# Kernel optimization log

Hardware: AMD Instinct MI355X
Metric: run time of the kernel (lower is better)

Reference implementation:

```python
import jax, jax.numpy as jnp
import numpy as np

N_NODES = 50000
N_EDGES = 800000
NFEAT = 512
NHID = 64
NHEADS = 8
NCLASS = 40
ALPHA = 0.2  # LeakyReLU slope
EPS = 1e-16  # guards isolated-node division


def setup_inputs() -> dict:
    key = jax.random.key(0)
    k = jax.random.split(key, 6)
    x = jax.random.normal(k[0], (N_NODES, NFEAT), dtype=jnp.float32)
    W_heads = jax.random.normal(k[1], (NHEADS, NFEAT, NHID), dtype=jnp.float32) * 0.05
    a_heads = jax.random.normal(k[2], (NHEADS, 2 * NHID), dtype=jnp.float32) * 0.05
    W_out = jax.random.normal(k[3], (NHEADS * NHID, NCLASS), dtype=jnp.float32) * 0.05
    a_out = jax.random.normal(k[4], (2 * NCLASS,), dtype=jnp.float32) * 0.05
    edge_index = jax.random.randint(k[5], (2, N_EDGES), 0, N_NODES, dtype=jnp.int32)
    return {"x": x, "W_heads": W_heads, "a_heads": a_heads,
            "W_out": W_out, "a_out": a_out, "edge_index": edge_index}


def _gat_layer(x, W, a, row, col, concat):
    # pyGAT sparse layer: h = xW; e_ij = exp(-LeakyReLU(a^T [h_i || h_j]));
    # out_i = sum_j e_ij h_j / sum_j e_ij   (aggregate into row, gather from col)
    D = W.shape[1]
    h = x @ W                                            # [N, D]
    score = h[row] @ a[:D] + h[col] @ a[D:]              # [E]
    e = jnp.exp(-jax.nn.leaky_relu(score, ALPHA))        # [E]
    num = jax.ops.segment_sum(e[:, None] * h[col], row, num_segments=x.shape[0])  # [N, D]
    den = jax.ops.segment_sum(e, row, num_segments=x.shape[0])                    # [N]
    out = num / (den[:, None] + EPS)
    return jax.nn.elu(out) if concat else out


def reference(x, W_heads, a_heads, W_out, a_out, edge_index):
    # dropout layers are identity in eval mode (training=False)
    row, col = edge_index[0], edge_index[1]
    heads = jax.vmap(lambda W, a: _gat_layer(x, W, a, row, col, True))(W_heads, a_heads)
    # [H, N, D] -> [N, H*D] (concat along feature dim, head-major like torch.cat)
    hcat = jnp.transpose(heads, (1, 0, 2)).reshape(x.shape[0], -1)
    return _gat_layer(hcat, W_out, a_out, row, col, False)  # [N, NCLASS]
```

## Files before the change

kernel.cpp:

```cpp
#include <hip/hip_runtime.h>
#include <hip/hip_bf16.h>

#define N_NODES 50000
#define N_EDGES 800000
#define NFEAT   512
#define NHID    64
#define NHEADS  8
#define NCLASS  40
#define HD      (NHEADS*NHID)
#define ALPHA   0.2f
#define EPS_F   1e-16f
#define NCHUNK  ((N_NODES + 255)/256)

typedef __attribute__((ext_vector_type(8))) short short8;
typedef __attribute__((ext_vector_type(4))) float floatx4;

__device__ __forceinline__ float bf2f(unsigned short u) {
    union { unsigned int i; float f; } v; v.i = ((unsigned int)u) << 16; return v.f;
}
__device__ __forceinline__ unsigned short f2bf(float f) {
    union { __hip_bfloat16 h; unsigned short u; } cv;
    cv.h = __float2bfloat16(f);
    return cv.u;
}

__global__ void prep(const float* __restrict__ Wh, unsigned short* __restrict__ Wrb,
                     const float* __restrict__ Wo, unsigned short* __restrict__ Wob,
                     int* __restrict__ deg) {
    int idx = blockIdx.x*256 + threadIdx.x;
    if (idx >= 512*512) return;
    if (idx < N_NODES) deg[idx] = 0;
    {
        int n = idx >> 9, k = idx & 511;
        int hd = n >> 6, d = n & 63;
        Wrb[idx] = f2bf(Wh[(size_t)hd*NFEAT*NHID + (size_t)k*NHID + d]);
    }
    if (idx < 64*512) {
        int n = idx >> 9, k = idx & 511;
        float v = (n < NCLASS) ? Wo[(size_t)k*NCLASS + n] : 0.f;
        Wob[idx] = f2bf(v);
    }
}

__global__ __launch_bounds__(512, 4) void mfma_gemm1(const float* __restrict__ A,
                                                  const unsigned short* __restrict__ Bbf,
                                                  const float* __restrict__ a_heads,
                                                  unsigned short* __restrict__ H1p,
                                                  float* __restrict__ srcdot,
                                                  float* __restrict__ dstdot, int M) {
    int id = blockIdx.x;
    int rb = (id >> 5)*8 + (id & 7);
    int cb = (id >> 3) & 3;
    int row0 = rb * 128, col0 = cb * 128;
    if (row0 >= M) return;

    __shared__ short Asl[128*40];
    __shared__ short Bsl[128*40];
    int tid  = threadIdx.x;
    int wid  = tid >> 6, lane = tid & 63;
    int lrow = lane & 15, quad = lane >> 4;
    int wm = wid >> 1, wn = wid & 1;

    int sr = tid >> 2, sk = (tid & 3) * 8;
    int ar = row0 + sr;
    int arow = ar < M ? ar : M - 1;

    floatx4 acc[2][4];
#pragma unroll
    for (int mm = 0; mm < 2; mm++)
#pragma unroll
        for (int nn = 0; nn < 4; nn++) acc[mm][nn] = (floatx4){0.f,0.f,0.f,0.f};

    float4 fa0, fa1;
    short8 fb;
    {
        const float* src = A + (size_t)arow*512 + sk;
        fa0 = *(const float4*)src;
        fa1 = *(const float4*)(src + 4);
        fb  = *(const short8*)(Bbf + (size_t)(col0 + sr)*512 + sk);
    }

    for (int k0 = 0; k0 < 512; k0 += 32) {
        {
            short8 h;
            h[0] = (short)f2bf(fa0.x); h[1] = (short)f2bf(fa0.y);
            h[2] = (short)f2bf(fa0.z); h[3] = (short)f2bf(fa0.w);
            h[4] = (short)f2bf(fa1.x); h[5] = (short)f2bf(fa1.y);
            h[6] = (short)f2bf(fa1.z); h[7] = (short)f2bf(fa1.w);
            *(short8*)(&Asl[sr*40 + sk]) = h;
            *(short8*)(&Bsl[sr*40 + sk]) = fb;
        }
        __syncthreads();
        if (k0 + 32 < 512) {
            int kn = k0 + 32;
            const float* src = A + (size_t)arow*512 + kn + sk;
            fa0 = *(const float4*)src;
            fa1 = *(const float4*)(src + 4);
            fb  = *(const short8*)(Bbf + (size_t)(col0 + sr)*512 + kn + sk);
        }
        short8 af[2], bfr[4];
#pragma unroll
        for (int mm = 0; mm < 2; ++mm)
            af[mm] = *(const short8*)(&Asl[(wm*32 + mm*16 + lrow)*40 + quad*8]);
#pragma unroll
        for (int nn = 0; nn < 4; ++nn)
            bfr[nn] = *(const short8*)(&Bsl[(wn*64 + nn*16 + lrow)*40 + quad*8]);
#pragma unroll
        for (int mm = 0; mm < 2; ++mm)
#pragma unroll
            for (int nn = 0; nn < 4; ++nn)
                acc[mm][nn] = __builtin_amdgcn_mfma_f32_16x16x32_bf16(
                    af[mm], bfr[nn], acc[mm][nn], 0, 0, 0);
        __syncthreads();
    }

    {
        int head = (col0 >> 6) + wn;
        float a0v[4], a1v[4];
#pragma unroll
        for (int nn = 0; nn < 4; ++nn) {
            a0v[nn] = a_heads[head*128 + nn*16 + lrow];
            a1v[nn] = a_heads[head*128 + 64 + nn*16 + lrow];
        }
#pragma unroll
        for (int mm = 0; mm < 2; ++mm) {
#pragma unroll
            for (int r = 0; r < 4; ++r) {
                float s0 = 0.f, s1 = 0.f;
#pragma unroll
                for (int nn = 0; nn < 4; ++nn) {
                    float v = acc[mm][nn][r];
                    s0 = fmaf(v, a0v[nn], s0);
                    s1 = fmaf(v, a1v[nn], s1);
                }
#pragma unroll
                for (int off = 1; off < 16; off <<= 1) {
                    s0 += __shfl_xor(s0, off, 64);
                    s1 += __shfl_xor(s1, off, 64);
                }
                int grow = row0 + wm*32 + mm*16 + quad*4 + r;
                if (lrow == 0 && grow < M) {
                    srcdot[(size_t)grow*8 + head] = s0;
                    dstdot[(size_t)grow*8 + head] = s1;
                }
            }
        }
    }

#pragma unroll
    for (int mm = 0; mm < 2; ++mm) {
        int rbase = row0 + wm*32 + mm*16 + quad*4;
#pragma unroll
        for (int nn = 0; nn < 4; ++nn) {
            int c = col0 + wn*64 + nn*16 + lrow;
            int off = (c & 63)*8 + (c >> 6);
#pragma unroll
            for (int r = 0; r < 4; ++r) {
                int grow = rbase + r;
                if (grow < M)
                    H1p[(size_t)grow*512 + off] = f2bf(acc[mm][nn][r]);
            }
        }
    }
}

__global__ __launch_bounds__(512, 4) void mfma_gemm2(const unsigned short* __restrict__ Abf,
                                                  const unsigned short* __restrict__ Bbf,
                                                  const float* __restrict__ a_out,
                                                  float* __restrict__ H2p,
                                                  float* __restrict__ src2,
                                                  float* __restrict__ dst2, int M) {
    __shared__ short Asl[128*40];
    __shared__ short Bsl[64*40];
    int tid  = threadIdx.x;
    int wid  = tid >> 6, lane = tid & 63;
    int lrow = lane & 15, quad = lane >> 4;
    int row0 = blockIdx.x * 128;
    if (row0 >= M) return;

    int sr = tid >> 2, sk = (tid & 3) * 8;
    int ar = row0 + sr; ar = ar < M ? ar : M - 1;
    int sr2 = (tid & 255) >> 2, sk2 = (tid & 3) * 8;

    floatx4 acc[4];
#pragma unroll
    for (int nn = 0; nn < 4; nn++) acc[nn] = (floatx4){0.f,0.f,0.f,0.f};

    short8 fa, fbv;
    fa = *(const short8*)(Abf + (size_t)ar*512 + sk);
    if (tid < 256)
        fbv = *(const short8*)(Bbf + (size_t)sr2*512 + sk2);

    for (int k0 = 0; k0 < 512; k0 += 32) {
        *(short8*)(&Asl[sr*40 + sk]) = fa;
        if (tid < 256)
            *(short8*)(&Bsl[sr2*40 + sk2]) = fbv;
        __syncthreads();
        if (k0 + 32 < 512) {
            int kn = k0 + 32;
            fa = *(const short8*)(Abf + (size_t)ar*512 + kn + sk);
            if (tid < 256)
                fbv = *(const short8*)(Bbf + (size_t)sr2*512 + kn + sk2);
        }
        short8 af, bfr[4];
        af = *(const short8*)(&Asl[(wid*16 + lrow)*40 + quad*8]);
#pragma unroll
        for (int nn = 0; nn < 4; ++nn)
            bfr[nn] = *(const short8*)(&Bsl[(nn*16 + lrow)*40 + quad*8]);
#pragma unroll
        for (int nn = 0; nn < 4; ++nn)
            acc[nn] = __builtin_amdgcn_mfma_f32_16x16x32_bf16(
                af, bfr[nn], acc[nn], 0, 0, 0);
        __syncthreads();
    }

    {
        float a0v[4], a1v[4];
#pragma unroll
        for (int nn = 0; nn < 4; ++nn) {
            int c = nn*16 + lrow;
            a0v[nn] = c < NCLASS ? a_out[c] : 0.f;
            a1v[nn] = c < NCLASS ? a_out[NCLASS + c] : 0.f;
        }
#pragma unroll
        for (int r = 0; r < 4; ++r) {
            float s0 = 0.f, s1 = 0.f;
#pragma unroll
            for (int nn = 0; nn < 4; ++nn) {
                float v = acc[nn][r];
                s0 = fmaf(v, a0v[nn], s0);
                s1 = fmaf(v, a1v[nn], s1);
            }
#pragma unroll
            for (int off = 1; off < 16; off <<= 1) {
                s0 += __shfl_xor(s0, off, 64);
                s1 += __shfl_xor(s1, off, 64);
            }
            int grow = row0 + wid*16 + quad*4 + r;
            if (lrow == 0 && grow < M) {
                src2[grow] = s0;
                dst2[grow] = s1;
            }
        }
    }

#pragma unroll
    for (int nn = 0; nn < 4; ++nn) {
        int c = nn*16 + lrow;
#pragma unroll
        for (int r = 0; r < 4; ++r) {
            int grow = row0 + wid*16 + quad*4 + r;
            if (grow < M)
                H2p[(size_t)grow*64 + c] = acc[nn][r];
        }
    }
}

__global__ void histk(const int* __restrict__ row, int* __restrict__ deg) {
    int e = blockIdx.x*256 + threadIdx.x;
    if (e < N_EDGES) atomicAdd(&deg[row[e]], 1);
}
__global__ void scanA(const int* __restrict__ deg, int* __restrict__ row_ptr,
                      int* __restrict__ chunk_tot) {
    __shared__ int s[256];
    int t = threadIdx.x;
    int idx = blockIdx.x*256 + t;
    int v = (idx < N_NODES) ? deg[idx] : 0;
    s[t] = v;
    __syncthreads();
#pragma unroll
    for (int off = 1; off < 256; off <<= 1) {
        int x = (t >= off) ? s[t-off] : 0;
        __syncthreads();
        s[t] += x;
        __syncthreads();
    }
    if (idx < N_NODES) row_ptr[idx] = s[t] - v;
    if (t == 255) chunk_tot[blockIdx.x] = s[t];
}
__global__ void scanB(const int* __restrict__ chunk_tot, int* __restrict__ chunk_off,
                      int* __restrict__ row_ptr) {
    __shared__ int s[256];
    int t = threadIdx.x;
    int v = (t < NCHUNK) ? chunk_tot[t] : 0;
    s[t] = v;
    __syncthreads();
#pragma unroll
    for (int off = 1; off < 256; off <<= 1) {
        int x = (t >= off) ? s[t-off] : 0;
        __syncthreads();
        s[t] += x;
        __syncthreads();
    }
    if (t < NCHUNK) chunk_off[t] = s[t] - v;
    if (t == 255) row_ptr[N_NODES] = s[t];
}
__global__ void scanC(const int* __restrict__ chunk_off, int* __restrict__ row_ptr,
                      int* __restrict__ cursor) {
    int idx = blockIdx.x*256 + threadIdx.x;
    if (idx < N_NODES) {
        int rp = row_ptr[idx] + chunk_off[idx >> 8];
        row_ptr[idx] = rp;
        cursor[idx] = rp;
    }
}

__global__ void fillk_w1(const int* __restrict__ row, const int* __restrict__ col,
                         const float* __restrict__ srcdot, const float* __restrict__ dstdot,
                         int* __restrict__ cursor, int* __restrict__ csr_col,
                         float* __restrict__ Wcsr) {
    int e = blockIdx.x*256 + threadIdx.x;
    if (e >= N_EDGES) return;
    int r = row[e], c = col[e];
    int pos = atomicAdd(&cursor[r], 1);
    csr_col[pos] = c;
    float4 sa = *(const float4*)(srcdot + (size_t)r*8);
    float4 sb = *(const float4*)(srcdot + (size_t)r*8 + 4);
    float4 da = *(const float4*)(dstdot + (size_t)c*8);
    float4 db = *(const float4*)(dstdot + (size_t)c*8 + 4);
    float s[8] = {sa.x+da.x, sa.y+da.y, sa.z+da.z, sa.w+da.w,
                  sb.x+db.x, sb.y+db.y, sb.z+db.z, sb.w+db.w};
    float o[8];
#pragma unroll
    for (int j = 0; j < 8; j++) {
        float lr = s[j] > 0.f ? s[j] : ALPHA*s[j];
        o[j] = __expf(-lr);
    }
    *(float4*)(Wcsr + (size_t)pos*8)     = make_float4(o[0], o[1], o[2], o[3]);
    *(float4*)(Wcsr + (size_t)pos*8 + 4) = make_float4(o[4], o[5], o[6], o[7]);
}

__global__ __launch_bounds__(256) void agg1(const unsigned short* __restrict__ H1p,
                                            const float* __restrict__ Wcsr,
                                            const int* __restrict__ row_ptr,
                                            const int* __restrict__ csr_col,
                                            unsigned short* __restrict__ hcatb) {
    int wave = (blockIdx.x*256 + threadIdx.x) >> 6;
    int lane = threadIdx.x & 63;
    if (wave >= N_NODES) return;
    int start = row_ptr[wave], end = row_ptr[wave+1];
    float acc[8], den[8];
#pragma unroll
    for (int j = 0; j < 8; j++) { acc[j] = 0.f; den[j] = 0.f; }

    int k = start;
    for (; k + 4 <= end; k += 4) {
        int c0 = csr_col[k],   c1 = csr_col[k+1];
        int c2 = csr_col[k+2], c3 = csr_col[k+3];
        short8 hv0 = *(const short8*)(H1p + (size_t)c0*512 + lane*8);
        short8 hv1 = *(const short8*)(H1p + (size_t)c1*512 + lane*8);
        short8 hv2 = *(const short8*)(H1p + (size_t)c2*512 + lane*8);
        short8 hv3 = *(const short8*)(H1p + (size_t)c3*512 + lane*8);
        float4 wv[8];
#pragma unroll
        for (int q = 0; q < 8; q++)
            wv[q] = *(const float4*)(Wcsr + (size_t)k*8 + q*4);
        const float* w0 = (const float*)&wv[0];
        const float* w1 = (const float*)&wv[2];
        const float* w2 = (const float*)&wv[4];
        const float* w3 = (const float*)&wv[6];
#pragma unroll
        for (int j = 0; j < 8; j++) {
            den[j] += (w0[j] + w1[j]) + (w2[j] + w3[j]);
            acc[j] = fmaf(w0[j], bf2f((unsigned short)hv0[j]), acc[j]);
            acc[j] = fmaf(w1[j], bf2f((unsigned short)hv1[j]), acc[j]);
            acc[j] = fmaf(w2[j], bf2f((unsigned short)hv2[j]), acc[j]);
            acc[j] = fmaf(w3[j], bf2f((unsigned short)hv3[j]), acc[j]);
        }
    }
    for (; k < end; ++k) {
        int c = csr_col[k];
        float4 wa = *(const float4*)(Wcsr + (size_t)k*8);
        float4 wb = *(const float4*)(Wcsr + (size_t)k*8 + 4);
        short8 hv = *(const short8*)(H1p + (size_t)c*512 + lane*8);
        float w[8] = {wa.x, wa.y, wa.z, wa.w, wb.x, wb.y, wb.z, wb.w};
#pragma unroll
        for (int j = 0; j < 8; j++) {
            den[j] += w[j];
            acc[j] = fmaf(w[j], bf2f((unsigned short)hv[j]), acc[j]);
        }
    }
#pragma unroll
    for (int j = 0; j < 8; j++) {
        float o = acc[j] / (den[j] + EPS_F);
        o = o > 0.f ? o : (__expf(o) - 1.f);
        hcatb[(size_t)wave*HD + j*64 + lane] = f2bf(o);
    }
}

__global__ __launch_bounds__(256) void agg2(const float* __restrict__ H2p,
                                            const float* __restrict__ src2,
                                            const float* __restrict__ dst2,
                                            const int* __restrict__ row_ptr,
                                            const int* __restrict__ csr_col,
                                            float* __restrict__ out) {
    int wave = (blockIdx.x*256 + threadIdx.x) >> 6;
    int lane = threadIdx.x & 63;
    if (wave >= N_NODES) return;
    int start = row_ptr[wave], end = row_ptr[wave+1];
    int deg = end - start;
    float s2i = src2[wave];
    int l = lane < NCLASS ? lane : 0;
    float acc = 0.f, den = 0.f;

    int colreg = 0;
    if (deg > 0) colreg = csr_col[start + (lane < deg ? lane : deg - 1)];

#define AG2_G1(T, H, IDX) do { \
    int cg_ = __builtin_amdgcn_readlane(colreg, (IDX)); \
    T = dst2[cg_]; \
    H = H2p[(size_t)cg_*64 + l]; \
} while(0)
#define AG2_C1(T, H) do { \
    float t_ = s2i + (T); \
    t_ = t_ > 0.f ? t_ : ALPHA*t_; \
    float w_ = __expf(-t_); \
    den += w_; acc = fmaf(w_, (H), acc); \
} while(0)
#define AG2_G8(T0,T1,T2,T3,T4,T5,T6,T7,H0,H1,H2,H3,H4,H5,H6,H7,BASE) do { \
    AG2_G1(T0,H0,(BASE));   AG2_G1(T1,H1,(BASE)+1); \
    AG2_G1(T2,H2,(BASE)+2); AG2_G1(T3,H3,(BASE)+3); \
    AG2_G1(T4,H4,(BASE)+4); AG2_G1(T5,H5,(BASE)+5); \
    AG2_G1(T6,H6,(BASE)+6); AG2_G1(T7,H7,(BASE)+7); \
} while(0)
#define AG2_C8(T0,T1,T2,T3,T4,T5,T6,T7,H0,H1,H2,H3,H4,H5,H6,H7) do { \
    AG2_C1(T0,H0); AG2_C1(T1,H1); AG2_C1(T2,H2); AG2_C1(T3,H3); \
    AG2_C1(T4,H4); AG2_C1(T5,H5); AG2_C1(T6,H6); AG2_C1(T7,H7); \
} while(0)

    int lim = deg < 64 ? deg : 64;
    int nb = lim >> 3;
    int k = start;
    float ta0,ta1,ta2,ta3,ta4,ta5,ta6,ta7, ga0,ga1,ga2,ga3,ga4,ga5,ga6,ga7;
    float tb0,tb1,tb2,tb3,tb4,tb5,tb6,tb7, gb0,gb1,gb2,gb3,gb4,gb5,gb6,gb7;
    if (nb > 0) {
        AG2_G8(ta0,ta1,ta2,ta3,ta4,ta5,ta6,ta7, ga0,ga1,ga2,ga3,ga4,ga5,ga6,ga7, 0);
        int b = 1;
        for (; b + 1 < nb; b += 2) {
            AG2_G8(tb0,tb1,tb2,tb3,tb4,tb5,tb6,tb7, gb0,gb1,gb2,gb3,gb4,gb5,gb6,gb7, b*8);
            AG2_C8(ta0,ta1,ta2,ta3,ta4,ta5,ta6,ta7, ga0,ga1,ga2,ga3,ga4,ga5,ga6,ga7);
            AG2_G8(ta0,ta1,ta2,ta3,ta4,ta5,ta6,ta7, ga0,ga1,ga2,ga3,ga4,ga5,ga6,ga7, (b+1)*8);
            AG2_C8(tb0,tb1,tb2,tb3,tb4,tb5,tb6,tb7, gb0,gb1,gb2,gb3,gb4,gb5,gb6,gb7);
        }
        if (b < nb) {
            AG2_G8(tb0,tb1,tb2,tb3,tb4,tb5,tb6,tb7, gb0,gb1,gb2,gb3,gb4,gb5,gb6,gb7, b*8);
            AG2_C8(ta0,ta1,ta2,ta3,ta4,ta5,ta6,ta7, ga0,ga1,ga2,ga3,ga4,ga5,ga6,ga7);
            AG2_C8(tb0,tb1,tb2,tb3,tb4,tb5,tb6,tb7, gb0,gb1,gb2,gb3,gb4,gb5,gb6,gb7);
        } else {
            AG2_C8(ta0,ta1,ta2,ta3,ta4,ta5,ta6,ta7, ga0,ga1,ga2,ga3,ga4,ga5,ga6,ga7);
        }
        k = start + nb*8;
    }
    for (; k < end; ++k) {
        int c_ = (k - start < 64) ? __builtin_amdgcn_readlane(colreg, k - start)
                                  : csr_col[k];
        float t = dst2[c_];
        float h = H2p[(size_t)c_*64 + l];
        AG2_C1(t, h);
    }
#undef AG2_G1
#undef AG2_C1
#undef AG2_G8
#undef AG2_C8

    if (lane < NCLASS)
        out[(size_t)wave*NCLASS + lane] = acc / (den + EPS_F);
}

extern "C" void kernel_launch(void* const* d_in, const int* in_sizes, int n_in,
                              void* d_out, int out_size, void* d_ws, size_t ws_size,
                              hipStream_t stream) {
    const float* x       = (const float*)d_in[0];
    const float* W_heads = (const float*)d_in[1];
    const float* a_heads = (const float*)d_in[2];
    const float* W_out   = (const float*)d_in[3];
    const float* a_out   = (const float*)d_in[4];
    const int*   ei      = (const int*)d_in[5];
    const int*   row     = ei;
    const int*   col     = ei + N_EDGES;
    float* out = (float*)d_out;

    char* ws = (char*)d_ws;
    size_t off = 0;
    auto alloc = [&](size_t bytes) {
        char* p = ws + off;
        off = (off + bytes + 255) & ~(size_t)255;
        return p;
    };
    unsigned short* Wrb   = (unsigned short*)alloc((size_t)512*512*2);
    unsigned short* Wob   = (unsigned short*)alloc((size_t)64*512*2);
    unsigned short* H1p   = (unsigned short*)alloc((size_t)N_NODES*HD*2);
    unsigned short* hcatb = (unsigned short*)alloc((size_t)N_NODES*HD*2);
    float* srcdot  = (float*)alloc((size_t)N_NODES*NHEADS*4);
    float* dstdot  = (float*)alloc((size_t)N_NODES*NHEADS*4);
    float* Wcsr    = (float*)alloc((size_t)N_EDGES*NHEADS*4);
    int*   deg     = (int*)alloc((size_t)N_NODES*4);
    int*   row_ptr = (int*)alloc((size_t)(N_NODES+1)*4);
    int*   cursor  = (int*)alloc((size_t)N_NODES*4);
    int*   ctot    = (int*)alloc(256*4);
    int*   coff    = (int*)alloc(256*4);
    int*   csr_col = (int*)alloc((size_t)N_EDGES*4);
    float* H2p     = (float*)alloc((size_t)N_NODES*64*4);
    float* src2    = (float*)alloc((size_t)N_NODES*4);
    float* dst2    = (float*)alloc((size_t)N_NODES*4);
    (void)ws_size;

    const int EB = (N_EDGES + 255)/256;
    const int WB = (N_NODES*64 + 255)/256;

    prep<<<(512*512 + 255)/256, 256, 0, stream>>>(W_heads, Wrb, W_out, Wob, deg);
    {
        int rtiles = (N_NODES + 127)/128;
        int nblk = ((rtiles + 7)/8) * 32;
        mfma_gemm1<<<nblk, 512, 0, stream>>>(x, Wrb, a_heads, H1p,
                                             srcdot, dstdot, N_NODES);
    }

    histk<<<EB, 256, 0, stream>>>(row, deg);
    scanA<<<NCHUNK, 256, 0, stream>>>(deg, row_ptr, ctot);
    scanB<<<1, 256, 0, stream>>>(ctot, coff, row_ptr);
    scanC<<<NCHUNK, 256, 0, stream>>>(coff, row_ptr, cursor);
    fillk_w1<<<EB, 256, 0, stream>>>(row, col, srcdot, dstdot, cursor,
                                     csr_col, Wcsr);

    agg1<<<WB, 256, 0, stream>>>(H1p, Wcsr, row_ptr, csr_col, hcatb);

    mfma_gemm2<<<(N_NODES + 127)/128, 512, 0, stream>>>(hcatb, Wob, a_out,
                                                        H2p, src2, dst2, N_NODES);
    agg2<<<WB, 256, 0, stream>>>(H2p, src2, dst2, row_ptr, csr_col, out);
}
```

Before: 498.7 us.

## Pre-convert x to bf16 and stage GEMM tiles via direct global-to-LDS loads

Adds a separate kernel that converts x to bf16 once, so gemm1 reads bf16 instead of converting fp32 inside its inner loop. Both GEMMs now load tiles straight into LDS with global_load_lds instead of staging through registers, dropping the padded LDS stride and the register prefetch. gemm1 moves to 256 threads with a 4x4 MFMA tile per wave, and the bf16 x buffer is reused as hcatb. The cost is an extra pass over x, the loss of global/compute overlap within an iteration, and possible LDS bank conflicts from the unpadded stride.

```diff
diff --git a/kernel.cpp b/kernel.cpp
--- a/kernel.cpp
+++ b/kernel.cpp
@@ -24,6 +24,27 @@
     return cv.u;
 }
 
+__device__ __forceinline__ void gload16(const unsigned short* g, short* l) {
+    __builtin_amdgcn_global_load_lds(
+        (const __attribute__((address_space(1))) void*)g,
+        (__attribute__((address_space(3))) void*)l,
+        16, 0, 0);
+}
+
+__global__ __launch_bounds__(256) void convx(const float* __restrict__ x,
+                                             unsigned short* __restrict__ xb) {
+    int i = blockIdx.x*256 + threadIdx.x;
+    if (i >= N_NODES*64) return;
+    const float* s = x + (size_t)i*8;
+    float4 a = *(const float4*)s, b = *(const float4*)(s+4);
+    short8 h;
+    h[0] = (short)f2bf(a.x); h[1] = (short)f2bf(a.y);
+    h[2] = (short)f2bf(a.z); h[3] = (short)f2bf(a.w);
+    h[4] = (short)f2bf(b.x); h[5] = (short)f2bf(b.y);
+    h[6] = (short)f2bf(b.z); h[7] = (short)f2bf(b.w);
+    *(short8*)(xb + (size_t)i*8) = h;
+}
+
 __global__ void prep(const float* __restrict__ Wh, unsigned short* __restrict__ Wrb,
                      const float* __restrict__ Wo, unsigned short* __restrict__ Wob,
                      int* __restrict__ deg) {
@@ -42,7 +63,7 @@
     }
 }
 
-__global__ __launch_bounds__(512, 4) void mfma_gemm1(const float* __restrict__ A,
+__global__ __launch_bounds__(256) void mfma_gemm1(const unsigned short* __restrict__ Abf,
                                                   const unsigned short* __restrict__ Bbf,
                                                   const float* __restrict__ a_heads,
                                                   unsigned short* __restrict__ H1p,
@@ -54,59 +75,47 @@
     int row0 = rb * 128, col0 = cb * 128;
     if (row0 >= M) return;
 
-    __shared__ short Asl[128*40];
-    __shared__ short Bsl[128*40];
+    __shared__ short Asl[128*32];
+    __shared__ short Bsl[128*32];
     int tid  = threadIdx.x;
     int wid  = tid >> 6, lane = tid & 63;
     int lrow = lane & 15, quad = lane >> 4;
-    int wm = wid >> 1, wn = wid & 1;
-
-    int sr = tid >> 2, sk = (tid & 3) * 8;
-    int ar = row0 + sr;
-    int arow = ar < M ? ar : M - 1;
-
-    floatx4 acc[2][4];
-#pragma unroll
-    for (int mm = 0; mm < 2; mm++)
+    int wm = wid & 1, wn = wid >> 1;
+
+    int srow = wid*16 + (lane >> 2);
+    int skk  = (lane & 3) * 8;
+    int ar0 = row0 + srow;      ar0 = ar0 < M ? ar0 : M - 1;
+    int ar1 = row0 + 64 + srow; ar1 = ar1 < M ? ar1 : M - 1;
+    const unsigned short* ag0 = Abf + (size_t)ar0*512 + skk;
+    const unsigned short* ag1 = Abf + (size_t)ar1*512 + skk;
+    const unsigned short* bg0 = Bbf + (size_t)(col0 + srow)*512 + skk;
+    const unsigned short* bg1 = Bbf + (size_t)(col0 + 64 + srow)*512 + skk;
+    short* al0 = &Asl[(wid*16)*32];
+    short* al1 = &Asl[(64 + wid*16)*32];
+    short* bl0 = &Bsl[(wid*16)*32];
+    short* bl1 = &Bsl[(64 + wid*16)*32];
+
+    floatx4 acc[4][4];
+#pragma unroll
+    for (int mm = 0; mm < 4; mm++)
 #pragma unroll
         for (int nn = 0; nn < 4; nn++) acc[mm][nn] = (floatx4){0.f,0.f,0.f,0.f};
 
-    float4 fa0, fa1;
-    short8 fb;
-    {
-        const float* src = A + (size_t)arow*512 + sk;
-        fa0 = *(const float4*)src;
-        fa1 = *(const float4*)(src + 4);
-        fb  = *(const short8*)(Bbf + (size_t)(col0 + sr)*512 + sk);
-    }
-
     for (int k0 = 0; k0 < 512; k0 += 32) {
-        {
-            short8 h;
-            h[0] = (short)f2bf(fa0.x); h[1] = (short)f2bf(fa0.y);
-            h[2] = (short)f2bf(fa0.z); h[3] = (short)f2bf(fa0.w);
-            h[4] = (short)f2bf(fa1.x); h[5] = (short)f2bf(fa1.y);
-            h[6] = (short)f2bf(fa1.z); h[7] = (short)f2bf(fa1.w);
-            *(short8*)(&Asl[sr*40 + sk]) = h;
-            *(short8*)(&Bsl[sr*40 + sk]) = fb;
-        }
-        __syncthreads();
-        if (k0 + 32 < 512) {
-            int kn = k0 + 32;
-            const float* src = A + (size_t)arow*512 + kn + sk;
-            fa0 = *(const float4*)src;
-            fa1 = *(const float4*)(src + 4);
-            fb  = *(const short8*)(Bbf + (size_t)(col0 + sr)*512 + kn + sk);
-        }
-        short8 af[2], bfr[4];
-#pragma unroll
-        for (int mm = 0; mm < 2; ++mm)
-            af[mm] = *(const short8*)(&Asl[(wm*32 + mm*16 + lrow)*40 + quad*8]);
+        gload16(ag0 + k0, al0);
+        gload16(ag1 + k0, al1);
+        gload16(bg0 + k0, bl0);
+        gload16(bg1 + k0, bl1);
+        __syncthreads();
+        short8 af[4], bfr[4];
+#pragma unroll
+        for (int mm = 0; mm < 4; ++mm)
+            af[mm] = *(const short8*)(&Asl[(wm*64 + mm*16 + lrow)*32 + quad*8]);
 #pragma unroll
         for (int nn = 0; nn < 4; ++nn)
-            bfr[nn] = *(const short8*)(&Bsl[(wn*64 + nn*16 + lrow)*40 + quad*8]);
-#pragma unroll
-        for (int mm = 0; mm < 2; ++mm)
+            bfr[nn] = *(const short8*)(&Bsl[(wn*64 + nn*16 + lrow)*32 + quad*8]);
+#pragma unroll
+        for (int mm = 0; mm < 4; ++mm)
 #pragma unroll
             for (int nn = 0; nn < 4; ++nn)
                 acc[mm][nn] = __builtin_amdgcn_mfma_f32_16x16x32_bf16(
@@ -123,7 +132,7 @@
             a1v[nn] = a_heads[head*128 + 64 + nn*16 + lrow];
         }
 #pragma unroll
-        for (int mm = 0; mm < 2; ++mm) {
+        for (int mm = 0; mm < 4; ++mm) {
 #pragma unroll
             for (int r = 0; r < 4; ++r) {
                 float s0 = 0.f, s1 = 0.f;
@@ -138,7 +147,7 @@
                     s0 += __shfl_xor(s0, off, 64);
                     s1 += __shfl_xor(s1, off, 64);
                 }
-                int grow = row0 + wm*32 + mm*16 + quad*4 + r;
+                int grow = row0 + wm*64 + mm*16 + quad*4 + r;
                 if (lrow == 0 && grow < M) {
                     srcdot[(size_t)grow*8 + head] = s0;
                     dstdot[(size_t)grow*8 + head] = s1;
@@ -148,8 +157,8 @@
     }
 
 #pragma unroll
-    for (int mm = 0; mm < 2; ++mm) {
-        int rbase = row0 + wm*32 + mm*16 + quad*4;
+    for (int mm = 0; mm < 4; ++mm) {
+        int rbase = row0 + wm*64 + mm*16 + quad*4;
 #pragma unroll
         for (int nn = 0; nn < 4; ++nn) {
             int c = col0 + wn*64 + nn*16 + lrow;
@@ -164,49 +173,41 @@
     }
 }
 
-__global__ __launch_bounds__(512, 4) void mfma_gemm2(const unsigned short* __restrict__ Abf,
+__global__ __launch_bounds__(512) void mfma_gemm2(const unsigned short* __restrict__ Abf,
                                                   const unsigned short* __restrict__ Bbf,
                                                   const float* __restrict__ a_out,
                                                   float* __restrict__ H2p,
                                                   float* __restrict__ src2,
                                                   float* __restrict__ dst2, int M) {
-    __shared__ short Asl[128*40];
-    __shared__ short Bsl[64*40];
+    __shared__ short Asl[128*32];
+    __shared__ short Bsl[64*32];
     int tid  = threadIdx.x;
     int wid  = tid >> 6, lane = tid & 63;
     int lrow = lane & 15, quad = lane >> 4;
     int row0 = blockIdx.x * 128;
     if (row0 >= M) return;
 
-    int sr = tid >> 2, sk = (tid & 3) * 8;
-    int ar = row0 + sr; ar = ar < M ? ar : M - 1;
-    int sr2 = (tid & 255) >> 2, sk2 = (tid & 3) * 8;
+    int srow = wid*16 + (lane >> 2);
+    int skk  = (lane & 3) * 8;
+    int ar = row0 + srow; ar = ar < M ? ar : M - 1;
+    const unsigned short* ag = Abf + (size_t)ar*512 + skk;
+    const unsigned short* bg = Bbf + (size_t)srow*512 + skk;
+    short* al = &Asl[(wid*16)*32];
+    short* bl = &Bsl[(wid*16)*32];
 
     floatx4 acc[4];
 #pragma unroll
     for (int nn = 0; nn < 4; nn++) acc[nn] = (floatx4){0.f,0.f,0.f,0.f};
 
-    short8 fa, fbv;
-    fa = *(const short8*)(Abf + (size_t)ar*512 + sk);
-    if (tid < 256)
-        fbv = *(const short8*)(Bbf + (size_t)sr2*512 + sk2);
-
     for (int k0 = 0; k0 < 512; k0 += 32) {
-        *(short8*)(&Asl[sr*40 + sk]) = fa;
-        if (tid < 256)
-            *(short8*)(&Bsl[sr2*40 + sk2]) = fbv;
-        __syncthreads();
-        if (k0 + 32 < 512) {
-            int kn = k0 + 32;
-            fa = *(const short8*)(Abf + (size_t)ar*512 + kn + sk);
-            if (tid < 256)
-                fbv = *(const short8*)(Bbf + (size_t)sr2*512 + kn + sk2);
-        }
+        gload16(ag + k0, al);
+        if (wid < 4) gload16(bg + k0, bl);
+        __syncthreads();
         short8 af, bfr[4];
-        af = *(const short8*)(&Asl[(wid*16 + lrow)*40 + quad*8]);
+        af = *(const short8*)(&Asl[(wid*16 + lrow)*32 + quad*8]);
 #pragma unroll
         for (int nn = 0; nn < 4; ++nn)
-            bfr[nn] = *(const short8*)(&Bsl[(nn*16 + lrow)*40 + quad*8]);
+            bfr[nn] = *(const short8*)(&Bsl[(nn*16 + lrow)*32 + quad*8]);
 #pragma unroll
         for (int nn = 0; nn < 4; ++nn)
             acc[nn] = __builtin_amdgcn_mfma_f32_16x16x32_bf16(
@@ -490,7 +491,8 @@
     unsigned short* Wrb   = (unsigned short*)alloc((size_t)512*512*2);
     unsigned short* Wob   = (unsigned short*)alloc((size_t)64*512*2);
     unsigned short* H1p   = (unsigned short*)alloc((size_t)N_NODES*HD*2);
-    unsigned short* hcatb = (unsigned short*)alloc((size_t)N_NODES*HD*2);
+    unsigned short* xb    = (unsigned short*)alloc((size_t)N_NODES*NFEAT*2);
+    unsigned short* hcatb = xb;
     float* srcdot  = (float*)alloc((size_t)N_NODES*NHEADS*4);
     float* dstdot  = (float*)alloc((size_t)N_NODES*NHEADS*4);
     float* Wcsr    = (float*)alloc((size_t)N_EDGES*NHEADS*4);
@@ -509,10 +511,11 @@
     const int WB = (N_NODES*64 + 255)/256;
 
     prep<<<(512*512 + 255)/256, 256, 0, stream>>>(W_heads, Wrb, W_out, Wob, deg);
+    convx<<<(N_NODES*64 + 255)/256, 256, 0, stream>>>(x, xb);
     {
         int rtiles = (N_NODES + 127)/128;
         int nblk = ((rtiles + 7)/8) * 32;
-        mfma_gemm1<<<nblk, 512, 0, stream>>>(x, Wrb, a_heads, H1p,
+        mfma_gemm1<<<nblk, 256, 0, stream>>>(xb, Wrb, a_heads, H1p,
                                              srcdot, dstdot, N_NODES);
     }
 
```

After: 509.0 us. 1.02x slower.
